# Kernel optimization log

Hardware: AMD Instinct MI355X
Metric: run time of the kernel (lower is better)

## Reference

```python
import jax, jax.numpy as jnp
import numpy as np

B, S, D, H = 4, 2048, 1024, 16
DH = D // H


def setup_inputs() -> dict:
    key = jax.random.key(0)
    k1, k2, k3, k4, k5 = jax.random.split(key, 5)
    x = jax.random.normal(k1, (B, S, D), dtype=jnp.float32)
    mask = jnp.tril(jnp.ones((S, S), dtype=bool))  # causal mask
    scale = 1.0 / np.sqrt(D)
    w_qkv = jax.random.normal(k2, (D, 3 * D), dtype=jnp.float32) * scale
    b_qkv = jnp.zeros((3 * D,), dtype=jnp.float32)
    w_out = jax.random.normal(k3, (D, D), dtype=jnp.float32) * scale
    b_out = jnp.zeros((D,), dtype=jnp.float32)
    return {"x": x, "w_qkv": w_qkv, "b_qkv": b_qkv, "w_out": w_out, "b_out": b_out, "mask": mask}


def reference(x, w_qkv, b_qkv, w_out, b_out, mask):
    qkv = jnp.einsum('bsd,de->bse', x, w_qkv) + b_qkv  # (B,S,3D)
    q, k, v = jnp.split(qkv, 3, axis=-1)
    # (B,S,D) -> (B,H,S,DH)
    q = q.reshape(B, S, H, DH).transpose(0, 2, 1, 3)
    k = k.reshape(B, S, H, DH).transpose(0, 2, 1, 3)
    v = v.reshape(B, S, H, DH).transpose(0, 2, 1, 3)
    scores = jnp.einsum('bhqd,bhkd->bhqk', q, k) / jnp.sqrt(jnp.float32(DH))
    scores = jnp.where(mask[None, None, :, :], scores, -jnp.inf)
    attn = jax.nn.softmax(scores, axis=-1)  # dropout p=0.0 -> identity
    out = jnp.einsum('bhqk,bhkd->bhqd', attn, v)
    out = out.transpose(0, 2, 1, 3).reshape(B, S, D)
    return jnp.einsum('bsd,de->bse', out, w_out) + b_out
```

## Files before the change

### kernel.cpp

```cpp
#include <hip/hip_runtime.h>
#include <hip/hip_bf16.h>

typedef unsigned short u16;
typedef __bf16 bf16x8 __attribute__((ext_vector_type(8)));
typedef float f32x4 __attribute__((ext_vector_type(4)));
typedef unsigned short u16x8 __attribute__((ext_vector_type(8)));

__device__ __forceinline__ void async_copy16(void* lds, const void* g) {
  __builtin_amdgcn_global_load_lds(
      (const __attribute__((address_space(1))) unsigned int*)g,
      (__attribute__((address_space(3))) unsigned int*)lds, 16, 0, 0);
}

__device__ __forceinline__ u16 f2bf(float f) {
  __hip_bfloat16 h = __float2bfloat16(f);
  u16 u;
  __builtin_memcpy(&u, &h, 2);
  return u;
}

__device__ __forceinline__ u16 f2bf_rne(float f) {
  unsigned b = __builtin_bit_cast(unsigned, f);
  b += 0x7FFF + ((b >> 16) & 1);
  return (u16)(b >> 16);
}

__device__ __forceinline__ unsigned cvt_pk_bf16(float a, float b) {
  unsigned r;
  asm("v_cvt_pk_bf16_f32 %0, %1, %2" : "=v"(r) : "v"(a), "v"(b));
  return r;
}

__global__ void k_f32_to_bf16(const float* __restrict__ in, u16* __restrict__ out, int n4) {
  int i = blockIdx.x * blockDim.x + threadIdx.x;
  if (i >= n4) return;
  float4 v = ((const float4*)in)[i];
  ushort4 o;
  o.x = f2bf(v.x); o.y = f2bf(v.y); o.z = f2bf(v.z); o.w = f2bf(v.w);
  ((ushort4*)out)[i] = o;
}

__global__ void k_transpose_bf16(const float* __restrict__ in, u16* __restrict__ out, int R, int C) {
  __shared__ float tile[32][33];
  int bx = blockIdx.x * 32;
  int by = blockIdx.y * 32;
  int tx = threadIdx.x & 31, ty = threadIdx.x >> 5;
  for (int i = ty; i < 32; i += 8) tile[i][tx] = in[(size_t)(by + i) * C + bx + tx];
  __syncthreads();
  for (int i = ty; i < 32; i += 8) out[(size_t)(bx + i) * R + by + tx] = f2bf(tile[tx][i]);
}

template <int OUT_BF16>
__global__ __launch_bounds__(256, 3) void k_gemm_bt(
    const u16* __restrict__ A, const u16* __restrict__ Bt,
    const float* __restrict__ bias, void* __restrict__ Cout,
    int M, int N, int K) {
  __shared__ __align__(16) u16 As[3][128][32];
  __shared__ __align__(16) u16 Bs[3][128][32];
  const int t = threadIdx.x;
  const int l = t & 63, w = t >> 6;
  const int lr = l & 15, lk = l >> 4;
  const int wr = w >> 1, wc = w & 1;
  const int m0 = blockIdx.x * 128, n0 = blockIdx.y * 128;
  const int nk = K >> 5;

  auto stage = [&](int kt) {
    int buf = kt - (kt / 3) * 3;
    int k0 = kt * 32;
#pragma unroll
    for (int c = 0; c < 2; ++c) {
      int idx = c * 256 + t;
      int row = idx >> 2, slot = idx & 3;
      int sw = (slot ^ ((row >> 1) & 3)) << 3;
      async_copy16((char*)&As[buf][0][0] + idx * 16, A + (size_t)(m0 + row) * K + k0 + sw);
      async_copy16((char*)&Bs[buf][0][0] + idx * 16, Bt + (size_t)(n0 + row) * K + k0 + sw);
    }
  };

  f32x4 acc[4][4] = {};

  stage(0);
  stage(1);
  asm volatile("s_waitcnt vmcnt(4)" ::: "memory");
  asm volatile("s_barrier" ::: "memory");

  for (int kt = 0; kt < nk; ++kt) {
    const int buf = kt - (kt / 3) * 3;
    if (kt + 2 < nk) stage(kt + 2);

    bf16x8 af[4], bfr[4];
#pragma unroll
    for (int m = 0; m < 4; ++m) {
      int row = wr * 64 + m * 16 + lr;
      af[m] = *(const bf16x8*)((const char*)&As[buf][0][0] + row * 64 + ((lk ^ ((row >> 1) & 3)) << 4));
    }
#pragma unroll
    for (int n = 0; n < 4; ++n) {
      int row = wc * 64 + n * 16 + lr;
      bfr[n] = *(const bf16x8*)((const char*)&Bs[buf][0][0] + row * 64 + ((lk ^ ((row >> 1) & 3)) << 4));
    }
#pragma unroll
    for (int m = 0; m < 4; ++m)
#pragma unroll
      for (int n = 0; n < 4; ++n)
        acc[m][n] = __builtin_amdgcn_mfma_f32_16x16x32_bf16(af[m], bfr[n], acc[m][n], 0, 0, 0);

    if (kt + 2 < nk) asm volatile("s_waitcnt vmcnt(4)" ::: "memory");
    else asm volatile("s_waitcnt vmcnt(0)" ::: "memory");
    asm volatile("s_barrier" ::: "memory");
  }

  for (int n = 0; n < 4; ++n) {
    int col = n0 + wc * 64 + n * 16 + lr;
    float bv = bias[col];
    for (int m = 0; m < 4; ++m) {
      int rowb = m0 + wr * 64 + m * 16 + lk * 4;
      for (int r = 0; r < 4; ++r) {
        float v = acc[m][n][r] + bv;
        size_t off = (size_t)(rowb + r) * N + col;
        if constexpr (OUT_BF16) ((u16*)Cout)[off] = f2bf(v);
        else ((float*)Cout)[off] = v;
      }
    }
  }
}

__global__ __launch_bounds__(256, 3) void k_attn(
    const u16* __restrict__ QKV,
    u16* __restrict__ O) {
  const int bh = blockIdx.x;
  const int qt = 15 - blockIdx.y;
  const int b = bh >> 4, h = bh & 15;
  const int t = threadIdx.x;
  const int l = t & 63, w = t >> 6;
  const int lr = l & 15, lk = l >> 4;
  constexpr float LG = 0.18033688f;

  __shared__ __align__(16) u16 Ks[2][64][64];
  __shared__ __align__(16) u16 VT[2][64][64];
  __shared__ __align__(16) u16 Pl[4][32][64];

  const u16* Kb0 = QKV + (size_t)b * 2048 * 3072 + 1024 + h * 64;
  const u16* Vb0 = Kb0 + 1024;

  u16x8 vreg[2];

  auto stageK = [&](int j, int buf) {
#pragma unroll
    for (int c = 0; c < 2; ++c) {
      int gi = c * 256 + t;
      int row = gi >> 3, slot = gi & 7;
      async_copy16((char*)&Ks[buf][0][0] + gi * 16,
                   Kb0 + ((size_t)j * 64 + row) * 3072 + ((slot ^ (row & 7)) << 3));
    }
  };
  auto loadV = [&](int j) {
#pragma unroll
    for (int c = 0; c < 2; ++c) {
      int r = c * 32 + (t >> 3), dh0 = (t & 7) << 3;
      vreg[c] = *(const u16x8*)(Vb0 + ((size_t)j * 64 + r) * 3072 + dh0);
    }
  };
  auto writeV = [&](int buf) {
#pragma unroll
    for (int c = 0; c < 2; ++c) {
      int r = c * 32 + (t >> 3), dh0 = (t & 7) << 3;
#pragma unroll
      for (int jj = 0; jj < 8; ++jj) {
        int dh = dh0 + jj;
        int phi = (dh & 7) ^ ((dh >> 3) & 7);
        VT[buf][dh][((((r >> 3) ^ phi) & 7) << 3) | (r & 7)] = vreg[c][jj];
      }
    }
  };

  const int nt = 2 * qt + 2;
  const int q0w = qt * 128 + w * 32;
  const size_t rowQ = (size_t)b * 2048 + q0w;

  bf16x8 qf[2][2];
#pragma unroll
  for (int g = 0; g < 2; ++g)
#pragma unroll
    for (int c = 0; c < 2; ++c)
      qf[g][c] = *(const bf16x8*)(QKV + (rowQ + g * 16 + lr) * 3072 + h * 64 + c * 32 + lk * 8);

  f32x4 acc[2][4] = {};
  float mi[2], li[2];
#pragma unroll
  for (int g = 0; g < 2; ++g) { mi[g] = -__builtin_inff(); li[g] = 0.f; }

  stageK(0, 0);
  loadV(0);
  writeV(0);
  __syncthreads();

  for (int j = 0; j < nt; ++j) {
    const int cur = j & 1;
    const bool more = (j + 1 < nt);
    if (more) { stageK(j + 1, cur ^ 1); loadV(j + 1); }

    f32x4 s[2][4] = {};
    __builtin_amdgcn_s_setprio(1);
#pragma unroll
    for (int c = 0; c < 2; ++c)
#pragma unroll
      for (int n = 0; n < 4; ++n) {
        int row = n * 16 + lr;
        bf16x8 kf = *(const bf16x8*)((const char*)&Ks[cur][0][0] + row * 128 +
                                     ((((c * 4 + lk) ^ (row & 7)) & 7) << 4));
        s[0][n] = __builtin_amdgcn_mfma_f32_16x16x32_bf16(kf, qf[0][c], s[0][n], 0, 0, 0);
        s[1][n] = __builtin_amdgcn_mfma_f32_16x16x32_bf16(kf, qf[1][c], s[1][n], 0, 0, 0);
      }
    __builtin_amdgcn_s_setprio(0);

    if (j * 64 + 63 > q0w) {
      const int kb = j * 64 + lk * 4;
#pragma unroll
      for (int g = 0; g < 2; ++g) {
        const int qq = q0w + g * 16 + lr;
#pragma unroll
        for (int n = 0; n < 4; ++n)
#pragma unroll
          for (int r = 0; r < 4; ++r)
            if (kb + n * 16 + r > qq) s[g][n][r] = -__builtin_inff();
      }
    }

    float tm[2];
#pragma unroll
    for (int g = 0; g < 2; ++g) {
      float m0 = fmaxf(fmaxf(s[g][0][0], s[g][0][1]), fmaxf(s[g][0][2], s[g][0][3]));
      float m1 = fmaxf(fmaxf(s[g][1][0], s[g][1][1]), fmaxf(s[g][1][2], s[g][1][3]));
      float m2 = fmaxf(fmaxf(s[g][2][0], s[g][2][1]), fmaxf(s[g][2][2], s[g][2][3]));
      float m3 = fmaxf(fmaxf(s[g][3][0], s[g][3][1]), fmaxf(s[g][3][2], s[g][3][3]));
      float x = fmaxf(fmaxf(m0, m1), fmaxf(m2, m3));
      x = fmaxf(x, __shfl_xor(x, 16));
      x = fmaxf(x, __shfl_xor(x, 32));
      tm[g] = x;
    }
    if (__any((tm[0] > mi[0] + 64.0f) || (tm[1] > mi[1] + 64.0f))) {
#pragma unroll
      for (int g = 0; g < 2; ++g) {
        float mnew = fmaxf(mi[g], tm[g]);
        float alpha = __builtin_amdgcn_exp2f((mi[g] - mnew) * LG);
        mi[g] = mnew;
        li[g] *= alpha;
        float a0 = __shfl(alpha, lk * 4 + 0);
        float a1 = __shfl(alpha, lk * 4 + 1);
        float a2 = __shfl(alpha, lk * 4 + 2);
        float a3 = __shfl(alpha, lk * 4 + 3);
#pragma unroll
        for (int n = 0; n < 4; ++n) {
          acc[g][n][0] *= a0; acc[g][n][1] *= a1; acc[g][n][2] *= a2; acc[g][n][3] *= a3;
        }
      }
    }

    u16* pw = &Pl[w][0][0];
#pragma unroll
    for (int g = 0; g < 2; ++g) {
      const float mc = -mi[g] * LG;
      float ps = 0.f;
#pragma unroll
      for (int n = 0; n < 4; ++n) {
        float p0 = __builtin_amdgcn_exp2f(fmaf(s[g][n][0], LG, mc));
        float p1 = __builtin_amdgcn_exp2f(fmaf(s[g][n][1], LG, mc));
        float p2 = __builtin_amdgcn_exp2f(fmaf(s[g][n][2], LG, mc));
        float p3 = __builtin_amdgcn_exp2f(fmaf(s[g][n][3], LG, mc));
        ps += (p0 + p1) + (p2 + p3);
        unsigned w0 = cvt_pk_bf16(p0, p1);
        unsigned w1 = cvt_pk_bf16(p2, p3);
        int kc = (n * 2 + (lk >> 1)) ^ (lr & 7);
        *(uint2*)(pw + (g * 16 + lr) * 64 + kc * 8 + (lk & 1) * 4) = make_uint2(w0, w1);
      }
      ps += __shfl_xor(ps, 16);
      ps += __shfl_xor(ps, 32);
      li[g] += ps;
    }

    __builtin_amdgcn_s_setprio(1);
#pragma unroll
    for (int c = 0; c < 2; ++c) {
      bf16x8 pa0 = *(const bf16x8*)(pw + lr * 64 + (((c * 4 + lk) ^ (lr & 7)) << 3));
      bf16x8 pa1 = *(const bf16x8*)(pw + (16 + lr) * 64 + (((c * 4 + lk) ^ (lr & 7)) << 3));
#pragma unroll
      for (int n = 0; n < 4; ++n) {
        int dh = n * 16 + lr;
        int phi = (dh & 7) ^ ((dh >> 3) & 7);
        bf16x8 vf = *(const bf16x8*)((const char*)&VT[cur][0][0] + dh * 128 +
                                     ((((c * 4 + lk) ^ phi) & 7) << 4));
        acc[0][n] = __builtin_amdgcn_mfma_f32_16x16x32_bf16(pa0, vf, acc[0][n], 0, 0, 0);
        acc[1][n] = __builtin_amdgcn_mfma_f32_16x16x32_bf16(pa1, vf, acc[1][n], 0, 0, 0);
      }
    }
    __builtin_amdgcn_s_setprio(0);

    if (more) writeV(cur ^ 1);
    __syncthreads();
  }

#pragma unroll
  for (int g = 0; g < 2; ++g) {
    float l0 = __shfl(li[g], lk * 4 + 0);
    float l1 = __shfl(li[g], lk * 4 + 1);
    float l2 = __shfl(li[g], lk * 4 + 2);
    float l3 = __shfl(li[g], lk * 4 + 3);
    float inv[4] = {1.0f / l0, 1.0f / l1, 1.0f / l2, 1.0f / l3};
#pragma unroll
    for (int r = 0; r < 4; ++r) {
      size_t orow = (rowQ + g * 16 + lk * 4 + r) * 1024 + h * 64;
#pragma unroll
      for (int n = 0; n < 4; ++n) O[orow + n * 16 + lr] = f2bf_rne(acc[g][n][r] * inv[r]);
    }
  }
}

extern "C" void kernel_launch(void* const* d_in, const int* in_sizes, int n_in,
                              void* d_out, int out_size, void* d_ws, size_t ws_size,
                              hipStream_t stream) {
  const float* x = (const float*)d_in[0];
  const float* w_qkv = (const float*)d_in[1];
  const float* b_qkv = (const float*)d_in[2];
  const float* w_out = (const float*)d_in[3];
  const float* b_out = (const float*)d_in[4];

  char* ws = (char*)d_ws;
  u16* X16 = (u16*)(ws);
  u16* WqkvT = (u16*)(ws + 16777216);
  u16* WoutT = (u16*)(ws + 23068672);
  u16* QKVb = (u16*)(ws + 25165824);
  u16* O16 = X16;

  k_f32_to_bf16<<<8192, 256, 0, stream>>>(x, X16, 8388608 / 4);
  k_transpose_bf16<<<dim3(96, 32), 256, 0, stream>>>(w_qkv, WqkvT, 1024, 3072);
  k_transpose_bf16<<<dim3(32, 32), 256, 0, stream>>>(w_out, WoutT, 1024, 1024);
  k_gemm_bt<1><<<dim3(64, 24), 256, 0, stream>>>(X16, WqkvT, b_qkv, QKVb, 8192, 3072, 1024);
  k_attn<<<dim3(64, 16), 256, 0, stream>>>(QKVb, O16);
  k_gemm_bt<0><<<dim3(64, 8), 256, 0, stream>>>(O16, WoutT, b_out, d_out, 8192, 1024, 1024);
}
```

Before: 175.8 us.

## Enlarge GEMM tiles to 256x128x64 with 512 threads and split-phase staging

Replaces the 128x128x32 bf16 GEMM with a 256x128 tile and a K step of 64, run by 8 waves per block. Each block reads its B tile once for twice as many rows, and the K loop has half as many barriers. Each K step is split into two phases that interleave async loads with MFMA work, with a new XOR swizzle and s_setprio raised around the MFMAs. The costs are a larger LDS footprint (144KB across three buffers), fewer blocks in the grid, and possible occupancy or tail effects on the output projection GEMM, which now launches only 256 blocks.

```diff
diff --git a/kernel.cpp b/kernel.cpp
--- a/kernel.cpp
+++ b/kernel.cpp
@@ -51,61 +51,71 @@
 }
 
 template <int OUT_BF16>
-__global__ __launch_bounds__(256, 3) void k_gemm_bt(
+__global__ __launch_bounds__(512, 2) void k_gemm256(
     const u16* __restrict__ A, const u16* __restrict__ Bt,
     const float* __restrict__ bias, void* __restrict__ Cout,
     int M, int N, int K) {
-  __shared__ __align__(16) u16 As[3][128][32];
-  __shared__ __align__(16) u16 Bs[3][128][32];
+  __shared__ __align__(16) u16 Asb[3][256][64];
+  __shared__ __align__(16) u16 Bsb[3][128][64];
   const int t = threadIdx.x;
   const int l = t & 63, w = t >> 6;
   const int lr = l & 15, lk = l >> 4;
   const int wr = w >> 1, wc = w & 1;
-  const int m0 = blockIdx.x * 128, n0 = blockIdx.y * 128;
-  const int nk = K >> 5;
-
-  auto stage = [&](int kt) {
+  const int m0 = blockIdx.x * 256, n0 = blockIdx.y * 128;
+  const int nk = K >> 6;
+
+  auto stage = [&](int kt, int half) {
     int buf = kt - (kt / 3) * 3;
-    int k0 = kt * 32;
-#pragma unroll
-    for (int c = 0; c < 2; ++c) {
-      int idx = c * 256 + t;
-      int row = idx >> 2, slot = idx & 3;
-      int sw = (slot ^ ((row >> 1) & 3)) << 3;
-      async_copy16((char*)&As[buf][0][0] + idx * 16, A + (size_t)(m0 + row) * K + k0 + sw);
-      async_copy16((char*)&Bs[buf][0][0] + idx * 16, Bt + (size_t)(n0 + row) * K + k0 + sw);
+    int k0 = kt * 64;
+#pragma unroll
+    for (int c = 0; c < 2; ++c) {
+      int gi = (half * 2 + c) * 512 + t;
+      int row = gi >> 3, slot = gi & 7;
+      async_copy16((char*)&Asb[buf][0][0] + gi * 16,
+                   A + (size_t)(m0 + row) * K + k0 + ((slot ^ (row & 7)) << 3));
+    }
+    {
+      int gi = half * 512 + t;
+      int row = gi >> 3, slot = gi & 7;
+      async_copy16((char*)&Bsb[buf][0][0] + gi * 16,
+                   Bt + (size_t)(n0 + row) * K + k0 + ((slot ^ (row & 7)) << 3));
     }
   };
 
   f32x4 acc[4][4] = {};
 
-  stage(0);
-  stage(1);
-  asm volatile("s_waitcnt vmcnt(4)" ::: "memory");
+  stage(0, 0); stage(0, 1);
+  stage(1, 0); stage(1, 1);
+  asm volatile("s_waitcnt vmcnt(6)" ::: "memory");
   asm volatile("s_barrier" ::: "memory");
 
   for (int kt = 0; kt < nk; ++kt) {
     const int buf = kt - (kt / 3) * 3;
-    if (kt + 2 < nk) stage(kt + 2);
-
-    bf16x8 af[4], bfr[4];
-#pragma unroll
-    for (int m = 0; m < 4; ++m) {
-      int row = wr * 64 + m * 16 + lr;
-      af[m] = *(const bf16x8*)((const char*)&As[buf][0][0] + row * 64 + ((lk ^ ((row >> 1) & 3)) << 4));
-    }
-#pragma unroll
-    for (int n = 0; n < 4; ++n) {
-      int row = wc * 64 + n * 16 + lr;
-      bfr[n] = *(const bf16x8*)((const char*)&Bs[buf][0][0] + row * 64 + ((lk ^ ((row >> 1) & 3)) << 4));
-    }
-#pragma unroll
-    for (int m = 0; m < 4; ++m)
-#pragma unroll
-      for (int n = 0; n < 4; ++n)
-        acc[m][n] = __builtin_amdgcn_mfma_f32_16x16x32_bf16(af[m], bfr[n], acc[m][n], 0, 0, 0);
-
-    if (kt + 2 < nk) asm volatile("s_waitcnt vmcnt(4)" ::: "memory");
+#pragma unroll
+    for (int ph = 0; ph < 2; ++ph) {
+      if (kt + 2 < nk) stage(kt + 2, ph);
+      bf16x8 af[4], bfr[4];
+#pragma unroll
+      for (int m = 0; m < 4; ++m) {
+        int rowL = wr * 64 + m * 16 + lr;
+        af[m] = *(const bf16x8*)((const char*)&Asb[buf][0][0] + rowL * 128 +
+                                 (((ph * 4 + lk) ^ (rowL & 7)) << 4));
+      }
+#pragma unroll
+      for (int n = 0; n < 4; ++n) {
+        int rowL = wc * 64 + n * 16 + lr;
+        bfr[n] = *(const bf16x8*)((const char*)&Bsb[buf][0][0] + rowL * 128 +
+                                  (((ph * 4 + lk) ^ (rowL & 7)) << 4));
+      }
+      __builtin_amdgcn_s_setprio(1);
+#pragma unroll
+      for (int m = 0; m < 4; ++m)
+#pragma unroll
+        for (int n = 0; n < 4; ++n)
+          acc[m][n] = __builtin_amdgcn_mfma_f32_16x16x32_bf16(af[m], bfr[n], acc[m][n], 0, 0, 0);
+      __builtin_amdgcn_s_setprio(0);
+    }
+    if (kt + 2 < nk) asm volatile("s_waitcnt vmcnt(6)" ::: "memory");
     else asm volatile("s_waitcnt vmcnt(0)" ::: "memory");
     asm volatile("s_barrier" ::: "memory");
   }
@@ -335,7 +345,7 @@
   k_f32_to_bf16<<<8192, 256, 0, stream>>>(x, X16, 8388608 / 4);
   k_transpose_bf16<<<dim3(96, 32), 256, 0, stream>>>(w_qkv, WqkvT, 1024, 3072);
   k_transpose_bf16<<<dim3(32, 32), 256, 0, stream>>>(w_out, WoutT, 1024, 1024);
-  k_gemm_bt<1><<<dim3(64, 24), 256, 0, stream>>>(X16, WqkvT, b_qkv, QKVb, 8192, 3072, 1024);
+  k_gemm256<1><<<dim3(32, 24), 512, 0, stream>>>(X16, WqkvT, b_qkv, QKVb, 8192, 3072, 1024);
   k_attn<<<dim3(64, 16), 256, 0, stream>>>(QKVb, O16);
-  k_gemm_bt<0><<<dim3(64, 8), 256, 0, stream>>>(O16, WoutT, b_out, d_out, 8192, 1024, 1024);
-}
+  k_gemm256<0><<<dim3(32, 8), 512, 0, stream>>>(O16, WoutT, b_out, d_out, 8192, 1024, 1024);
+}
```

Measured after the change: 191.4 us. 1.09x slower.
